# Kernel optimization log

Hardware: AMD Instinct MI355X
Metric: run time of the kernel (lower is better)

## Reference

```python
import jax, jax.numpy as jnp
import numpy as np

N, E, G = 50000, 800000, 64
H, C, EDIM = 4, 64, 16
NT, NR, NCLS = 8, 6, 2
NEG_SLOPE = 0.2


def setup_inputs() -> dict:
    key = jax.random.key(0)
    ks = jax.random.split(key, 24)
    d = {}
    d['node_type'] = jax.random.randint(ks[0], (N,), 0, NT, dtype=jnp.int32)
    d['edge_type'] = jax.random.randint(ks[1], (E,), 0, NR, dtype=jnp.int32)
    d['edge_index'] = jax.random.randint(ks[2], (2, E), 0, N, dtype=jnp.int32)
    d['batch'] = jnp.sort(jax.random.randint(ks[3], (N,), 0, G, dtype=jnp.int32))
    i = [4]
    def rn(shape, scale=0.1):
        a = jax.random.normal(ks[i[0]], shape, dtype=jnp.float32) * scale
        i[0] += 1
        return a
    d['node_emb'] = rn((NT, C))
    d['edge_emb'] = rn((NR, EDIM))
    for l in (0, 1):
        d[f'W{l}'] = rn((C, H * C))
        d[f'We{l}'] = rn((EDIM, H * C))
        d[f'att_src{l}'] = rn((H, C))
        d[f'att_dst{l}'] = rn((H, C))
        d[f'att_edge{l}'] = rn((H, C))
        d[f'b{l}'] = jnp.zeros((C,), jnp.float32)
    d['cw1'] = rn((C, C))
    d['cb1'] = jnp.zeros((C,), jnp.float32)
    d['cw2'] = rn((C, NCLS))
    d['cb2'] = jnp.zeros((NCLS,), jnp.float32)
    return d


def gat_layer(x, ea, src, dst, W, We, a_src, a_dst, a_edge, b):
    # x: [N, C], ea: [E, EDIM]
    h = (x @ W).reshape(N, H, C)          # transformed node features
    he = (ea @ We).reshape(E, H, C)       # transformed edge features
    # per-edge attention logits [E, H]
    alpha = ((h * a_src).sum(-1)[src]
             + (h * a_dst).sum(-1)[dst]
             + (he * a_edge).sum(-1))
    alpha = jax.nn.leaky_relu(alpha, NEG_SLOPE)
    # segment softmax over destination neighborhoods
    m = jax.ops.segment_max(alpha, dst, num_segments=N)
    alpha = jnp.exp(alpha - m[dst])
    den = jax.ops.segment_sum(alpha, dst, num_segments=N)
    alpha = alpha / (den[dst] + 1e-16)
    # weighted scatter-add of source features, then mean over heads
    out = jax.ops.segment_sum(alpha[:, :, None] * h[src], dst, num_segments=N)
    return jax.nn.elu(out.mean(axis=1) + b)


def reference(node_type, edge_type, edge_index, batch, node_emb, edge_emb,
              W0, We0, att_src0, att_dst0, att_edge0, b0,
              W1, We1, att_src1, att_dst1, att_edge1, b1,
              cw1, cb1, cw2, cb2):
    src, dst = edge_index[0], edge_index[1]
    x = node_emb[node_type]          # [N, C]
    ea = edge_emb[edge_type]         # [E, EDIM]
    x = gat_layer(x, ea, src, dst, W0, We0, att_src0, att_dst0, att_edge0, b0)
    x = gat_layer(x, ea, src, dst, W1, We1, att_src1, att_dst1, att_edge1, b1)
    # global mean pool over graphs
    s = jax.ops.segment_sum(x, batch, num_segments=G)
    cnt = jax.ops.segment_sum(jnp.ones((N, 1), x.dtype), batch, num_segments=G)
    g = s / jnp.maximum(cnt, 1.0)
    # classifier (dropout inactive in eval)
    return jax.nn.relu(g @ cw1 + cb1) @ cw2 + cb2
```

## Files before the change

### kernel.cpp

```cpp
#include <hip/hip_runtime.h>
#include <hip/hip_bf16.h>

#define N_NODES 50000
#define N_EDGES 800000
#define N_GRAPH 64
#define NHEAD 4
#define CDIM 64
#define HC 256
#define NTT 8
#define NRR 6
#define EDIMM 16
#define SCAN_CHUNK 1024
#define NBLK_SCAN ((N_NODES + SCAN_CHUNK - 1) / SCAN_CHUNK)
#define H1SCALE 1024.f

typedef unsigned short u16;
typedef unsigned char u8;
typedef __attribute__((ext_vector_type(8))) short bf8;
typedef __attribute__((ext_vector_type(4))) float f4;
typedef __attribute__((ext_vector_type(2))) float v2f;

__device__ __forceinline__ float eluf(float v) { return v > 0.f ? v : expm1f(v); }
__device__ __forceinline__ u16 f2u(float f) {
    union { float f; unsigned int i; } c; c.f = f;
    unsigned int i = c.i;
    return (u16)((i + 0x7FFFu + ((i >> 16) & 1u)) >> 16);
}
__device__ __forceinline__ float lrelu(float v) { return v > 0.f ? v : 0.2f * v; }
__device__ __forceinline__ u8 f2fp8(float v) {
    return (u8)(__builtin_amdgcn_cvt_pk_fp8_f32(v, 0.f, 0, false) & 0xFF);
}

__global__ __launch_bounds__(256) void k_zero(float* __restrict__ p, int n)
{
    int i = blockIdx.x * 256 + threadIdx.x;
    if (i < n) p[i] = 0.f;
}

__global__ __launch_bounds__(256) void k_tables(
    const float* __restrict__ node_emb, const float* __restrict__ edge_emb,
    const float* __restrict__ W0, const float* __restrict__ We0,
    const float* __restrict__ as0, const float* __restrict__ ad0,
    const float* __restrict__ ae0, const float* __restrict__ We1,
    const float* __restrict__ ae1,
    float* __restrict__ t_h0, float* __restrict__ t_as0,
    float* __restrict__ t_ad0, float* __restrict__ t_ae0,
    float* __restrict__ t_ae1)
{
    __shared__ float srow[HC];
    __shared__ float srow2[HC];
    int tid = threadIdx.x;
    int b = blockIdx.x;
    if (b < NTT) {
        int t = b;
        float acc = 0.f;
        #pragma unroll 8
        for (int k = 0; k < CDIM; k++)
            acc += node_emb[t * CDIM + k] * W0[k * HC + tid];
        srow[tid] = acc;
        t_h0[t * HC + tid] = acc;
        __syncthreads();
        if (tid < NHEAD) {
            int h = tid;
            float a = 0.f, d = 0.f;
            for (int c = 0; c < CDIM; c++) {
                float hv = srow[h * CDIM + c];
                a += hv * as0[h * CDIM + c];
                d += hv * ad0[h * CDIM + c];
            }
            t_as0[t * NHEAD + h] = a;
            t_ad0[t * NHEAD + h] = d;
        }
    } else {
        int r = b - NTT;
        float a0 = 0.f, a1 = 0.f;
        #pragma unroll
        for (int k = 0; k < EDIMM; k++) {
            float ev = edge_emb[r * EDIMM + k];
            a0 += ev * We0[k * HC + tid];
            a1 += ev * We1[k * HC + tid];
        }
        srow[tid] = a0;
        srow2[tid] = a1;
        __syncthreads();
        if (tid < NHEAD) {
            int h = tid;
            float s0 = 0.f, s1 = 0.f;
            for (int c = 0; c < CDIM; c++) {
                s0 += srow[h * CDIM + c] * ae0[h * CDIM + c];
                s1 += srow2[h * CDIM + c] * ae1[h * CDIM + c];
            }
            t_ae0[r * NHEAD + h] = s0;
            t_ae1[r * NHEAD + h] = s1;
        }
    }
}

__global__ __launch_bounds__(256) void k_count(
    const int* __restrict__ edge_index, int* __restrict__ deg4,
    const int* __restrict__ batch, int* __restrict__ goffs)
{
    int i = blockIdx.x * 256 + threadIdx.x;
    if (i < N_EDGES)
        atomicAdd(&deg4[(blockIdx.x & 3) * N_NODES + edge_index[N_EDGES + i]], 1);
    if (i < N_NODES) {
        int bi = batch[i];
        int bp = (i == 0) ? -1 : batch[i - 1];
        for (int g = bp + 1; g <= bi; g++) goffs[g] = i;
        if (i == N_NODES - 1)
            for (int g = bi + 1; g <= N_GRAPH; g++) goffs[g] = N_NODES;
    }
}

__global__ __launch_bounds__(256) void k_scan1(
    const int* __restrict__ deg4, int* __restrict__ deg, int* __restrict__ blksum,
    const float* __restrict__ t_as0, const float* __restrict__ t_ad0,
    const float* __restrict__ t_ae0, float* __restrict__ t_exp)
{
    __shared__ int s[256];
    int b = blockIdx.x, tid = threadIdx.x;
    int base = b * SCAN_CHUNK + tid * 4;
    int t = 0;
    #pragma unroll
    for (int k = 0; k < 4; k++) {
        int i = base + k;
        if (i < N_NODES) {
            int d = deg4[i] + deg4[N_NODES + i] + deg4[2 * N_NODES + i]
                  + deg4[3 * N_NODES + i];
            deg[i] = d;
            t += d;
        }
    }
    s[tid] = t;
    __syncthreads();
    for (int off = 128; off > 0; off >>= 1) {
        if (tid < off) s[tid] += s[tid + off];
        __syncthreads();
    }
    if (tid == 0) blksum[b] = s[0];
    if (b == 0) {
        for (int idx = tid; idx < NTT * NRR * NTT * NHEAD; idx += 256) {
            int tn = idx / 192;
            int rem = idx - tn * 192;
            int et = rem >> 5;
            int ts = (rem >> 2) & 7;
            int hq = idx & 3;
            float lg = t_as0[ts * NHEAD + hq] + t_ad0[tn * NHEAD + hq]
                     + t_ae0[et * NHEAD + hq];
            t_exp[idx] = __expf(lrelu(lg));
        }
    }
}

__global__ __launch_bounds__(256) void k_scan3(
    const int* __restrict__ deg, const int* __restrict__ blksum,
    int* __restrict__ offs, int* __restrict__ cursor)
{
    __shared__ int s[256];
    __shared__ int sbase;
    int b = blockIdx.x, tid = threadIdx.x;
    if (tid < 64) {
        int v = (tid < b) ? blksum[tid] : 0;
        #pragma unroll
        for (int d = 32; d >= 1; d >>= 1) v += __shfl_xor(v, d);
        if (tid == 0) sbase = v;
    }
    int base = b * SCAN_CHUNK + tid * 4;
    int d4[4]; int t = 0;
    #pragma unroll
    for (int k = 0; k < 4; k++) {
        int i = base + k;
        d4[k] = (i < N_NODES) ? deg[i] : 0;
        t += d4[k];
    }
    s[tid] = t;
    __syncthreads();
    for (int off = 1; off < 256; off <<= 1) {
        int v = (tid >= off) ? s[tid - off] : 0;
        __syncthreads();
        s[tid] += v;
        __syncthreads();
    }
    int excl = sbase + s[tid] - t;
    #pragma unroll
    for (int k = 0; k < 4; k++) {
        int i = base + k;
        if (i < N_NODES) { offs[i] = excl; cursor[i] = excl; }
        excl += d4[k];
    }
    if (b == NBLK_SCAN - 1 && tid == 255) offs[N_NODES] = excl;
}

__global__ __launch_bounds__(256) void k_scatter(
    const int* __restrict__ edge_index, const int* __restrict__ edge_type,
    const int* __restrict__ node_type, int* __restrict__ cursor,
    int* __restrict__ csrp)
{
    int e = blockIdx.x * 256 + threadIdx.x;
    if (e < N_EDGES) {
        int d  = edge_index[N_EDGES + e];
        int s  = edge_index[e];
        int et = edge_type[e];
        int ts = node_type[s];
        int pos = atomicAdd(&cursor[d], 1);
        csrp[pos] = s | (et << 16) | (ts << 19);
    }
}

__global__ __launch_bounds__(256) void k_layer0(
    const int* __restrict__ node_type, const int* __restrict__ offs,
    const int* __restrict__ csrp,
    const float* __restrict__ t_h0, const float* __restrict__ t_exp,
    const float* __restrict__ b0, u16* __restrict__ x1b)
{
    __shared__ float s_h0[NTT * HC];
    __shared__ float s_exp[NTT * NRR * NTT * NHEAD];
    __shared__ float s_b0[CDIM];
    __shared__ int   s_hist[4][64];
    __shared__ float s_w[4][32];
    __shared__ float s_den[4][4];

    int tid = threadIdx.x;
    {
        const float4* a = (const float4*)t_h0;
        float4* d = (float4*)s_h0;
        #pragma unroll
        for (int i = 0; i < 2; i++) d[tid + i * 256] = a[tid + i * 256];
        const float4* bsrc = (const float4*)t_exp;
        float4* e = (float4*)s_exp;
        #pragma unroll
        for (int i = 0; i < 3; i++) e[tid + i * 256] = bsrc[tid + i * 256];
        if (tid < CDIM) s_b0[tid] = b0[tid];
    }
    __syncthreads();

    int lane = tid & 63, wv = tid >> 6;
    int h = lane >> 4;
    int cq = (lane & 15) << 2;
    int hoff = h * CDIM + cq;
    int tsw = lane >> 2, hw = lane & 3;

    for (int it = 0; it < 4; it++) {
        int n = blockIdx.x * 16 + wv * 4 + it;
        int tn = node_type[n];
        int e0 = offs[n], e1 = offs[n + 1];
        s_hist[wv][lane] = 0;
        __syncthreads();
        for (int i = e0 + lane; i < e1; i += 64)
            atomicAdd(&s_hist[wv][(csrp[i] >> 16) & 63], 1);
        __syncthreads();
        float wsum = 0.f;
        if (lane < 32) {
            int base = tn * 192 + tsw * 4 + hw;
            #pragma unroll
            for (int et = 0; et < NRR; et++)
                wsum += (float)s_hist[wv][tsw * 8 + et] * s_exp[base + et * 32];
        }
        float den = wsum;
        den += __shfl_xor(den, 4);
        den += __shfl_xor(den, 8);
        den += __shfl_xor(den, 16);
        if (lane < 32) s_w[wv][lane] = wsum;
        if (lane < 4)  s_den[wv][lane] = den;
        __syncthreads();
        float ax = 0.f, ay = 0.f, az = 0.f, aw = 0.f;
        #pragma unroll
        for (int ts = 0; ts < NTT; ts++) {
            float wt = s_w[wv][ts * 4 + h];
            const float4 v = *(const float4*)(s_h0 + ts * HC + hoff);
            ax += wt * v.x; ay += wt * v.y; az += wt * v.z; aw += wt * v.w;
        }
        float inv = 0.25f / (s_den[wv][h] + 1e-16f);
        ax *= inv; ay *= inv; az *= inv; aw *= inv;
        ax += __shfl_xor(ax, 16); ax += __shfl_xor(ax, 32);
        ay += __shfl_xor(ay, 16); ay += __shfl_xor(ay, 32);
        az += __shfl_xor(az, 16); az += __shfl_xor(az, 32);
        aw += __shfl_xor(aw, 16); aw += __shfl_xor(aw, 32);
        if (lane < 16) {
            ushort4 o;
            o.x = f2u(eluf(ax + s_b0[cq + 0]));
            o.y = f2u(eluf(ay + s_b0[cq + 1]));
            o.z = f2u(eluf(az + s_b0[cq + 2]));
            o.w = f2u(eluf(aw + s_b0[cq + 3]));
            *(ushort4*)(x1b + (size_t)n * CDIM + cq) = o;
        }
    }
}

__global__ __launch_bounds__(256) void k_gemm1(
    const u16* __restrict__ x1b, const float* __restrict__ W1,
    const float* __restrict__ as1, const float* __restrict__ ad1,
    u8* __restrict__ h1f8, float* __restrict__ asrc1, float* __restrict__ adst1)
{
    __shared__ u8 ht[16 * HC];
    int tid = threadIdx.x;
    int lane = tid & 63, wv = tid >> 6;
    int quad = lane >> 4, c16 = lane & 15;

    bf8 bf[4][2];
    float sv[4], dv[4];
    #pragma unroll
    for (int t = 0; t < 4; t++) {
        int col = wv * 64 + t * 16 + c16;
        sv[t] = as1[col];
        dv[t] = ad1[col];
        #pragma unroll
        for (int kf = 0; kf < 2; kf++)
            #pragma unroll
            for (int j = 0; j < 8; j++)
                bf[t][kf][j] = (short)f2u(W1[(kf * 32 + quad * 8 + j) * HC + col]);
    }

    int nt = blockIdx.x;
    const bf8 a0 = *(const bf8*)(x1b + (size_t)(nt * 16 + c16) * CDIM + quad * 8);
    const bf8 a1 = *(const bf8*)(x1b + (size_t)(nt * 16 + c16) * CDIM + 32 + quad * 8);
    f4 acc[4];
    #pragma unroll
    for (int t = 0; t < 4; t++) {
        acc[t] = (f4){0.f, 0.f, 0.f, 0.f};
        acc[t] = __builtin_amdgcn_mfma_f32_16x16x32_bf16(a0, bf[t][0], acc[t], 0, 0, 0);
        acc[t] = __builtin_amdgcn_mfma_f32_16x16x32_bf16(a1, bf[t][1], acc[t], 0, 0, 0);
    }
    float rs[4] = {0.f, 0.f, 0.f, 0.f}, rd[4] = {0.f, 0.f, 0.f, 0.f};
    #pragma unroll
    for (int t = 0; t < 4; t++)
        #pragma unroll
        for (int reg = 0; reg < 4; reg++) {
            float v = acc[t][reg];
            rs[reg] += v * sv[t];
            rd[reg] += v * dv[t];
            ht[(quad * 4 + reg) * HC + wv * 64 + t * 16 + c16] = f2fp8(v * H1SCALE);
        }
    #pragma unroll
    for (int reg = 0; reg < 4; reg++)
        #pragma unroll
        for (int d = 1; d < 16; d <<= 1) {
            rs[reg] += __shfl_xor(rs[reg], d);
            rd[reg] += __shfl_xor(rd[reg], d);
        }
    if (c16 == 0) {
        #pragma unroll
        for (int reg = 0; reg < 4; reg++) {
            int nn = nt * 16 + quad * 4 + reg;
            asrc1[nn * NHEAD + wv] = rs[reg];
            adst1[nn * NHEAD + wv] = rd[reg];
        }
    }
    __syncthreads();
    const uint4* src = (const uint4*)ht;
    uint4* dst = (uint4*)(h1f8 + (size_t)nt * 16 * HC);
    dst[tid] = src[tid];
}

__global__ __launch_bounds__(256) void k_agg1(
    const int* __restrict__ offs, const int* __restrict__ csrp,
    const u8* __restrict__ h1f8, const float* __restrict__ asrc1,
    const float* __restrict__ adst1, const float* __restrict__ t_ae1,
    const float* __restrict__ b1, float* __restrict__ x2)
{
    __shared__ float s_ae[NRR * NHEAD];
    if (threadIdx.x < NRR * NHEAD) s_ae[threadIdx.x] = t_ae1[threadIdx.x];
    __syncthreads();

    int n = (blockIdx.x * 256 + threadIdx.x) >> 6;
    int lane = threadIdx.x & 63;
    int h = lane >> 4;
    int cq = (lane & 15) << 2;
    int q  = lane & 31;
    int ke = q >> 2;
    int hh = q & 3;
    float adst_hh = adst1[n * NHEAD + hh];

    int e0 = offs[n], e1 = offs[n + 1];
    int nb = (e1 - e0 + 7) >> 3;

    float ax = 0.f, ay = 0.f, az = 0.f, aw = 0.f, den = 0.f;

    int rec[8];
    if (nb > 0) {
        #pragma unroll
        for (int k = 0; k < 8; k++) {
            int idx = e0 + k; idx = idx < e1 ? idx : e1 - 1;
            rec[k] = csrp[idx];
        }
    }
    for (int b = 0; b < nb; b++) {
        int i = e0 + (b << 3);
        int lim = e1 - i;
        int s[8];
        #pragma unroll
        for (int k = 0; k < 8; k++) s[k] = rec[k] & 0xFFFF;
        int ete = (rec[ke] >> 16) & 7;
        float asve = asrc1[s[ke] * NHEAD + hh];
        unsigned int hw[8];
        #pragma unroll
        for (int k = 0; k < 8; k++)
            hw[k] = *(const unsigned int*)(h1f8 + (size_t)s[k] * HC + h * CDIM + cq);
        int ii = i + 8;
        #pragma unroll
        for (int k = 0; k < 8; k++) {
            int idx = ii + k; idx = idx < e1 ? idx : e1 - 1;
            rec[k] = csrp[idx];
        }
        float pe = __expf(lrelu(asve + adst_hh + s_ae[ete * NHEAD + hh]));
        #pragma unroll
        for (int k = 0; k < 8; k++) {
            float p = __shfl(pe, (k << 2) | h);
            p = (k < lim) ? p : 0.f;
            den += p;
            v2f lo = __builtin_amdgcn_cvt_pk_f32_fp8(hw[k], false);
            v2f hi = __builtin_amdgcn_cvt_pk_f32_fp8(hw[k], true);
            ax += p * lo.x; ay += p * lo.y;
            az += p * hi.x; aw += p * hi.y;
        }
    }
    float inv = (0.25f / H1SCALE) / (den + 1e-16f);
    ax *= inv; ay *= inv; az *= inv; aw *= inv;
    ax += __shfl_xor(ax, 16); ax += __shfl_xor(ax, 32);
    ay += __shfl_xor(ay, 16); ay += __shfl_xor(ay, 32);
    az += __shfl_xor(az, 16); az += __shfl_xor(az, 32);
    aw += __shfl_xor(aw, 16); aw += __shfl_xor(aw, 32);
    if (lane < 16) {
        float4 o;
        o.x = eluf(ax + b1[cq + 0]);
        o.y = eluf(ay + b1[cq + 1]);
        o.z = eluf(az + b1[cq + 2]);
        o.w = eluf(aw + b1[cq + 3]);
        *(float4*)(x2 + (size_t)n * CDIM + cq) = o;
    }
}

__global__ __launch_bounds__(256) void k_poolcls(
    const float* __restrict__ x2, const int* __restrict__ goffs,
    const float* __restrict__ cw1, const float* __restrict__ cb1,
    const float* __restrict__ cw2, const float* __restrict__ cb2,
    float* __restrict__ out, int wsMB,
    const int* __restrict__ offs, const int* __restrict__ csrp,
    const float* __restrict__ W1)
{
    __shared__ float part[4][CDIM];
    __shared__ float gsh[CDIM];
    int g = blockIdx.x;
    int ch = threadIdx.x & 63, rg = threadIdx.x >> 6;
    int gs = goffs[g], ge = goffs[g + 1];
    float acc = 0.f;
    for (int r = gs + rg; r < ge; r += 4)
        acc += x2[(size_t)r * CDIM + ch];
    part[rg][ch] = acc;
    __syncthreads();
    if (threadIdx.x < CDIM) {
        float s = part[0][ch] + part[1][ch] + part[2][ch] + part[3][ch];
        int c = ge - gs;
        gsh[ch] = s / (float)(c > 1 ? c : 1);
    }
    __syncthreads();
    if (threadIdx.x < 64) {
        int j = threadIdx.x;
        float a = cb1[j];
        #pragma unroll
        for (int k = 0; k < CDIM; k++) a += gsh[k] * cw1[k * CDIM + j];
        float hid = a > 0.f ? a : 0.f;
        float o0 = hid * cw2[j * 2 + 0];
        float o1 = hid * cw2[j * 2 + 1];
        #pragma unroll
        for (int d = 32; d >= 1; d >>= 1) {
            o0 += __shfl_xor(o0, d);
            o1 += __shfl_xor(o1, d);
        }
        if (j == 0) {
            out[g * 2 + 0] = o0 + cb2[0];
            out[g * 2 + 1] = o1 + cb2[1];
        }
    }
    if (g == 0) {
        __shared__ int simpl, soob, sA;
        if (threadIdx.x == 0) { simpl = 0; soob = 0; sA = 0; }
        __syncthreads();
        if (threadIdx.x == 0 && offs[N_NODES] != N_EDGES) atomicOr(&sA, 4);
        float v = W1[threadIdx.x];
        if (!(fabsf(v) < 100.f)) atomicAdd(&simpl, 1);
        int r = csrp[threadIdx.x];
        if ((r & 0xFFFF) >= N_NODES || (r >> 22) != 0 || r < 0) atomicAdd(&soob, 1);
        __syncthreads();
        if (threadIdx.x == 0) {
            int A = sA;
            if (simpl > 10) A |= 8;
            int B = soob > 1023 ? 1023 : soob;
            if (A | B) out[0] = (float)((A << 20) | (wsMB << 10) | B);
        }
    }
}

__global__ void k_fault(int code, float* __restrict__ out)
{
    if (threadIdx.x == 0 && blockIdx.x == 0) out[0] = (float)code;
}

extern "C" void kernel_launch(void* const* d_in, const int* in_sizes, int n_in,
                              void* d_out, int out_size, void* d_ws, size_t ws_size,
                              hipStream_t stream) {
    static const int rsize[22] = {50000, 800000, 1600000, 50000, 512, 96,
                                  16384, 4096, 256, 256, 256, 64,
                                  16384, 4096, 256, 256, 256, 64,
                                  4096, 64, 128, 2};
    static const int cand_pos[3][22] = {
        {21,19,18,12,20,17,0,2,8,4,6,10,1,3,9,5,7,11,15,13,16,14},
        {0,1,2,3,4,5,6,7,8,9,10,11,12,13,14,15,16,17,18,19,20,21},
        {17,15,14,8,16,13,18,20,4,0,2,6,19,21,5,1,3,7,11,9,12,10},
    };
    int mc = -1;
    if (n_in == 22) {
        for (int c = 0; c < 3 && mc < 0; c++) {
            bool ok = true;
            for (int r = 0; r < 22; r++)
                if (in_sizes[cand_pos[c][r]] != rsize[r]) { ok = false; break; }
            if (ok) mc = c;
        }
    }

    char* ws = (char*)d_ws;
    size_t off = 0;
    auto alloc = [&](size_t b) { size_t r = off; off += (b + 255) & ~(size_t)255; return r; };
    int*   deg4   = (int*)(ws + alloc((size_t)4 * N_NODES * 4));
    size_t zero_bytes = off;
    int*   deg    = (int*)(ws + alloc(N_NODES * 4));
    int*   blksum = (int*)(ws + alloc(NBLK_SCAN * 4));
    int*   offs   = (int*)(ws + alloc((N_NODES + 1) * 4));
    int*   cursor = (int*)(ws + alloc(N_NODES * 4));
    int*   csrp   = (int*)(ws + alloc(N_EDGES * 4));
    int*   goffs  = (int*)(ws + alloc((N_GRAPH + 1) * 4));
    float* t_h0   = (float*)(ws + alloc(NTT * HC * 4));
    float* t_as0  = (float*)(ws + alloc(NTT * NHEAD * 4));
    float* t_ad0  = (float*)(ws + alloc(NTT * NHEAD * 4));
    float* t_ae0  = (float*)(ws + alloc(NRR * NHEAD * 4));
    float* t_ae1  = (float*)(ws + alloc(NRR * NHEAD * 4));
    float* t_exp  = (float*)(ws + alloc(NTT * NRR * NTT * NHEAD * 4));
    u16*   x1b    = (u16*)(ws + alloc((size_t)N_NODES * CDIM * 2));
    float* asrc1  = (float*)(ws + alloc((size_t)N_NODES * NHEAD * 4));
    float* adst1  = (float*)(ws + alloc((size_t)N_NODES * NHEAD * 4));
    u8*    h1f8   = (u8*)(ws + alloc((size_t)N_NODES * HC));
    float* x2     = (float*)(ws + alloc((size_t)N_NODES * CDIM * 4));

    int wsMB = (int)(ws_size >> 20); if (wsMB > 1023) wsMB = 1023;
    int hostA = 0, hostB = 0;
    if (mc < 0) { hostA |= 1; hostB = (n_in != 22) ? (n_in < 1023 ? n_in : 1023) : 0; }
    if (mc >= 0 && off > ws_size) hostA |= 2;

    if (hostA == 0) {
        const int* P = cand_pos[mc];
        const int*   node_type  = (const int*)d_in[P[0]];
        const int*   edge_type  = (const int*)d_in[P[1]];
        const int*   edge_index = (const int*)d_in[P[2]];
        const int*   batch      = (const int*)d_in[P[3]];
        const float* node_emb   = (const float*)d_in[P[4]];
        const float* edge_emb   = (const float*)d_in[P[5]];
        const float* W0  = (const float*)d_in[P[6]];
        const float* We0 = (const float*)d_in[P[7]];
        const float* as0 = (const float*)d_in[P[8]];
        const float* ad0 = (const float*)d_in[P[9]];
        const float* ae0 = (const float*)d_in[P[10]];
        const float* b0  = (const float*)d_in[P[11]];
        const float* W1  = (const float*)d_in[P[12]];
        const float* We1 = (const float*)d_in[P[13]];
        const float* as1 = (const float*)d_in[P[14]];
        const float* ad1 = (const float*)d_in[P[15]];
        const float* ae1 = (const float*)d_in[P[16]];
        const float* b1  = (const float*)d_in[P[17]];
        const float* cw1 = (const float*)d_in[P[18]];
        const float* cb1 = (const float*)d_in[P[19]];
        const float* cw2 = (const float*)d_in[P[20]];
        const float* cb2 = (const float*)d_in[P[21]];

        int zero_elems = (int)(zero_bytes / 4);
        k_zero<<<(zero_elems + 255) / 256, 256, 0, stream>>>((float*)ws, zero_elems);
        k_tables<<<NTT + NRR, 256, 0, stream>>>(node_emb, edge_emb, W0, We0, as0,
                                                ad0, ae0, We1, ae1,
                                                t_h0, t_as0, t_ad0, t_ae0, t_ae1);
        k_count<<<(N_EDGES + 255) / 256, 256, 0, stream>>>(edge_index, deg4,
                                                           batch, goffs);
        k_scan1<<<NBLK_SCAN, 256, 0, stream>>>(deg4, deg, blksum,
                                               t_as0, t_ad0, t_ae0, t_exp);
        k_scan3<<<NBLK_SCAN, 256, 0, stream>>>(deg, blksum, offs, cursor);
        k_scatter<<<(N_EDGES + 255) / 256, 256, 0, stream>>>(edge_index, edge_type,
                                                             node_type, cursor, csrp);
        k_layer0<<<3125, 256, 0, stream>>>(
            node_type, offs, csrp, t_h0, t_exp, b0, x1b);
        k_gemm1<<<3125, 256, 0, stream>>>(
            x1b, W1, as1, ad1, h1f8, asrc1, adst1);
        k_agg1<<<(N_NODES * 64) / 256, 256, 0, stream>>>(
            offs, csrp, h1f8, asrc1, adst1, t_ae1, b1, x2);
        k_poolcls<<<N_GRAPH, 256, 0, stream>>>(
            x2, goffs, cw1, cb1, cw2, cb2, (float*)d_out, wsMB, offs, csrp, W1);
    } else {
        int code = (hostA << 20) | (wsMB << 10) | (hostB > 1023 ? 1023 : hostB);
        k_fault<<<1, 64, 0, stream>>>(code, (float*)d_out);
    }
}
```

Measured before the change: 329.5 us.

## Restructure layer-1 aggregation into wave-wide record load and double-buffered 16-edge volleys

For nodes with degree at most 64, the whole wave loads all CSR records in one coalesced read and distributes them by shuffle. It computes all attention weights up front, then gathers source features in 16-edge volleys into two register buffers so the next volley's loads overlap the current accumulation. The aim is fewer dependent load rounds and more memory-level parallelism per node than the serial 8-edge loop. The cost is higher register pressure and a kept fallback path for higher-degree nodes.

After: 359.5 us. 1.09x slower.

```diff
diff --git a/kernel.cpp b/kernel.cpp
--- a/kernel.cpp
+++ b/kernel.cpp
@@ -352,6 +352,28 @@
     dst[tid] = src[tid];
 }
 
+#define AGG_PROVIDE(AV, AE, C) { \
+    int rc_ = __shfl(myrec, ((C) << 4) + pr); \
+    AV = asrc1[((rc_ & 0xFFFF) << 2) + hh]; \
+    AE = s_ae[((rc_ >> 16) & 7) * NHEAD + hh]; }
+
+#define AGG_VOLLEY(HW, C) { \
+    _Pragma("unroll") \
+    for (int k = 0; k < 16; k++) { \
+        int rc_ = __shfl(myrec, ((C) << 4) + k); \
+        HW[k] = *(const unsigned int*)(h1p + ((size_t)(rc_ & 0xFFFF) << 8)); } }
+
+#define AGG_CONSUME(HW, PE, LIM) { \
+    _Pragma("unroll") \
+    for (int k = 0; k < 16; k++) { \
+        float p_ = __shfl((PE), (k << 2) | h); \
+        p_ = (k < (LIM)) ? p_ : 0.f; \
+        den += p_; \
+        v2f lo_ = __builtin_amdgcn_cvt_pk_f32_fp8(HW[k], false); \
+        v2f hi_ = __builtin_amdgcn_cvt_pk_f32_fp8(HW[k], true); \
+        ax += p_ * lo_.x; ay += p_ * lo_.y; \
+        az += p_ * hi_.x; aw += p_ * hi_.y; } }
+
 __global__ __launch_bounds__(256) void k_agg1(
     const int* __restrict__ offs, const int* __restrict__ csrp,
     const u8* __restrict__ h1f8, const float* __restrict__ asrc1,
@@ -366,52 +388,84 @@
     int lane = threadIdx.x & 63;
     int h = lane >> 4;
     int cq = (lane & 15) << 2;
-    int q  = lane & 31;
-    int ke = q >> 2;
-    int hh = q & 3;
-    float adst_hh = adst1[n * NHEAD + hh];
+    const u8* h1p = h1f8 + h * CDIM + cq;
+    int hh = lane & 3;
+    int pr = lane >> 2;
 
     int e0 = offs[n], e1 = offs[n + 1];
-    int nb = (e1 - e0 + 7) >> 3;
+    int deg = e1 - e0;
 
     float ax = 0.f, ay = 0.f, az = 0.f, aw = 0.f, den = 0.f;
 
-    int rec[8];
-    if (nb > 0) {
+    if (deg > 0 && deg <= 64) {
+        int idx = e0 + lane; idx = idx < e1 ? idx : e1 - 1;
+        int myrec = csrp[idx];
+        float adstq = adst1[(n << 2) + hh];
+        int nc = (deg + 15) >> 4;
+
+        float av0, ae0v, av1 = 0.f, ae1v = 0.f;
+        float av2 = 0.f, ae2v = 0.f, av3 = 0.f, ae3v = 0.f;
+        AGG_PROVIDE(av0, ae0v, 0);
+        if (nc > 1) AGG_PROVIDE(av1, ae1v, 1);
+        if (nc > 2) AGG_PROVIDE(av2, ae2v, 2);
+        if (nc > 3) AGG_PROVIDE(av3, ae3v, 3);
+
+        unsigned int hwA[16], hwB[16];
+        AGG_VOLLEY(hwA, 0);
+        if (nc > 1) AGG_VOLLEY(hwB, 1);
+
+        float pe0 = __expf(lrelu(av0 + ae0v + adstq));
+        float pe1 = (nc > 1) ? __expf(lrelu(av1 + ae1v + adstq)) : 0.f;
+        float pe2 = (nc > 2) ? __expf(lrelu(av2 + ae2v + adstq)) : 0.f;
+        float pe3 = (nc > 3) ? __expf(lrelu(av3 + ae3v + adstq)) : 0.f;
+
+        AGG_CONSUME(hwA, pe0, deg);
+        if (nc > 2) AGG_VOLLEY(hwA, 2);
+        if (nc > 1) AGG_CONSUME(hwB, pe1, deg - 16);
+        if (nc > 3) AGG_VOLLEY(hwB, 3);
+        if (nc > 2) AGG_CONSUME(hwA, pe2, deg - 32);
+        if (nc > 3) AGG_CONSUME(hwB, pe3, deg - 48);
+    } else if (deg > 64) {
+        int q = lane & 31;
+        int ke = q >> 2;
+        int hq = q & 3;
+        float adst_hh = adst1[(n << 2) + hq];
+        int nb = (deg + 7) >> 3;
+        int rec[8];
         #pragma unroll
         for (int k = 0; k < 8; k++) {
-            int idx = e0 + k; idx = idx < e1 ? idx : e1 - 1;
-            rec[k] = csrp[idx];
-        }
-    }
-    for (int b = 0; b < nb; b++) {
-        int i = e0 + (b << 3);
-        int lim = e1 - i;
-        int s[8];
-        #pragma unroll
-        for (int k = 0; k < 8; k++) s[k] = rec[k] & 0xFFFF;
-        int ete = (rec[ke] >> 16) & 7;
-        float asve = asrc1[s[ke] * NHEAD + hh];
-        unsigned int hw[8];
-        #pragma unroll
-        for (int k = 0; k < 8; k++)
-            hw[k] = *(const unsigned int*)(h1f8 + (size_t)s[k] * HC + h * CDIM + cq);
-        int ii = i + 8;
-        #pragma unroll
-        for (int k = 0; k < 8; k++) {
-            int idx = ii + k; idx = idx < e1 ? idx : e1 - 1;
-            rec[k] = csrp[idx];
-        }
-        float pe = __expf(lrelu(asve + adst_hh + s_ae[ete * NHEAD + hh]));
-        #pragma unroll
-        for (int k = 0; k < 8; k++) {
-            float p = __shfl(pe, (k << 2) | h);
-            p = (k < lim) ? p : 0.f;
-            den += p;
-            v2f lo = __builtin_amdgcn_cvt_pk_f32_fp8(hw[k], false);
-            v2f hi = __builtin_amdgcn_cvt_pk_f32_fp8(hw[k], true);
-            ax += p * lo.x; ay += p * lo.y;
-            az += p * hi.x; aw += p * hi.y;
+            int i2 = e0 + k; i2 = i2 < e1 ? i2 : e1 - 1;
+            rec[k] = csrp[i2];
+        }
+        for (int b = 0; b < nb; b++) {
+            int i = e0 + (b << 3);
+            int lim = e1 - i;
+            int s[8];
+            #pragma unroll
+            for (int k = 0; k < 8; k++) s[k] = rec[k] & 0xFFFF;
+            int ete = (rec[ke] >> 16) & 7;
+            float asve = asrc1[(s[ke] << 2) + hq];
+            unsigned int hw[8];
+            #pragma unroll
+            for (int k = 0; k < 8; k++)
+                hw[k] = *(const unsigned int*)(h1p + ((size_t)s[k] << 8));
+            int ii = i + 8;
+            #pragma unroll
+            for (int k = 0; k < 8; k++) {
+                int i2 = ii + k; i2 = i2 < e1 ? i2 : e1 - 1;
+                rec[k] = csrp[i2];
+            }
+            float pe = __expf(lrelu(asve + adst_hh + s_ae[ete * NHEAD + hq]));
+            #pragma unroll
+            for (int k = 0; k < 8; k++) {
+                float p = __shfl(pe, (k << 2) | h);
+                p = (k < lim) ? p : 0.f;
+                den += p;
+                v2f lo = __builtin_amdgcn_cvt_pk_f32_fp8(hw[k], false);
+                v2f hi = __builtin_amdgcn_cvt_pk_f32_fp8(hw[k], true);
+                ax += p * lo.x; ay += p * lo.y;
+                az += p * hi.x; aw += p * hi.y;
+            }
         }
     }
     float inv = (0.25f / H1SCALE) / (den + 1e-16f);
```
